# Kernel tuning notes

Hardware: AMD Instinct MI355X
Metric: run time of the kernel (lower is better)

The kernel has to match this reference:

```python
import jax, jax.numpy as jnp
import numpy as np
from itertools import permutations

# Static config (matches init_kwargs)
K = 4          # subgraph size; permdim P = (K-1)! = 6
H = 64         # hid_dim
B = 16         # number of graphs
N = 64         # nodes per graph (Nm == N)
SUBG_PER = 128 # subgraphs per graph
NS = B * SUBG_PER
OUT = 1
NREG = 4


def make_allperm(k):
    # all permutations of [1..k-1], with a 0 column prepended, transposed -> (k, P)
    perms = np.array(list(permutations(range(1, k))), dtype=np.int32)  # (P, k-1)
    allperm = np.concatenate([np.zeros((perms.shape[0], 1), np.int32), perms], axis=1)
    return jnp.asarray(allperm.T)  # (k, P)


def layer_norm(x, g, b, eps=1e-5):
    m = jnp.mean(x, axis=-1, keepdims=True)
    v = jnp.mean((x - m) ** 2, axis=-1, keepdims=True)
    return (x - m) / jnp.sqrt(v + eps) * g + b


def setup_inputs() -> dict:
    key = jax.random.key(0)
    ks = jax.random.split(key, 24)
    s = 1.0 / np.sqrt(H)
    # distinct node indices per subgraph: top-k of a random permutation
    r = jax.random.uniform(ks[2], (NS, N))
    subgs = jnp.argsort(r, axis=1)[:, :K].astype(jnp.int32)  # (NS, K)
    return {
        "x": jax.random.normal(ks[0], (B, N, 1), jnp.float32),
        "adj": (jax.random.uniform(ks[1], (B, N, N)) < 0.2).astype(jnp.float32),
        "subgs": subgs,
        "num_subg": jnp.full((B,), SUBG_PER, jnp.int32),
        # inmlp params (dead compute in original forward, kept for faithfulness)
        "in_w1": jax.random.normal(ks[3], (1, H)) * s,
        "in_b1": jnp.zeros((H,)),
        "in_w2": jax.random.normal(ks[4], (H, H)) * s,
        "in_b2": jnp.zeros((H,)),
        "in_ln_g": jnp.ones((H,)),
        "in_ln_b": jnp.zeros((H,)),
        "idemb": jax.random.normal(ks[5], (K + 2, H)) * 1.0,
        "id_w": jax.random.normal(ks[6], (H, H)) * s,
        "id_b": jnp.zeros((H,)),
        "set1_w": jax.random.normal(ks[7], (H, H)) * s,
        "set1_b": jnp.zeros((H,)),
        "set2_w": jax.random.normal(ks[8], (H, H)) * s,
        "set2_b": jnp.zeros((H,)),
        "reg_w1": jax.random.normal(ks[9], (NREG, H, H)) * s,
        "reg_b1": jnp.zeros((NREG, H)),
        "reg_w2": jax.random.normal(ks[10], (NREG, H, H)) * s,
        "reg_b2": jnp.zeros((NREG, H)),
        "reg_ln_g": jnp.ones((NREG, H)),
        "reg_ln_b": jnp.zeros((NREG, H)),
        "out_w": jax.random.normal(ks[11], (H, OUT)) * s,
        "out_b": jnp.zeros((OUT,)),
    }


def reference(x, adj, subgs, num_subg, in_w1, in_b1, in_w2, in_b2, in_ln_g, in_ln_b,
              idemb, id_w, id_b, set1_w, set1_b, set2_w, set2_b,
              reg_w1, reg_b1, reg_w2, reg_b2, reg_ln_g, reg_ln_b, out_w, out_b):
    b, n = adj.shape[0], adj.shape[-1]
    ns, k = subgs.shape
    h = idemb.shape[1]
    subgbatch = jnp.repeat(jnp.arange(b), num_subg, total_repeat_length=ns)  # (ns,)

    # inmlp (output is discarded by the original forward; only its shape is used)
    xe = jax.nn.relu(x @ in_w1 + in_b1)
    xe = jax.nn.relu(layer_norm(xe @ in_w2 + in_b2, in_ln_g, in_ln_b))
    del xe

    # node-id label injection: z[s, subgs[s, j], p, :] = emb(allperm[j, p]) * (j+1)*1000
    allperm = make_allperm(k)                                  # (k, P)
    p = allperm.shape[1]
    lab = idemb[allperm] * ((jnp.arange(k) + 1.0) * 1000.0)[:, None, None]  # (k, P, h)
    z = jnp.ones((ns, n, p, h), x.dtype)
    z = z.at[jnp.arange(ns)[:, None], subgs].set(jnp.broadcast_to(lab, (ns, k, p, h)))

    adj_ = adj[subgbatch]                                      # (ns, N, N)

    # id message-passing layer(s): z += SELU(Linear(A @ z)) ; num_layer_id = 1
    m = jnp.einsum('bij,bjpd->bipd', adj_, z)                  # (ns, N, P, h)
    z = z + jax.nn.selu(m @ id_w + id_b)

    z = jax.nn.selu(z.sum(axis=2) @ set1_w + set1_b)           # pool perms -> (ns, N, h)
    # num_layer_global = 0: no global message-passing layers
    g = jax.nn.selu(z.sum(axis=1) @ set2_w + set2_b)           # pool nodes -> (ns, h)
    g = jax.ops.segment_max(g, subgbatch, num_segments=b)      # global max pool -> (B, h)

    for i in range(reg_w1.shape[0]):
        t = jax.nn.relu(g @ reg_w1[i] + reg_b1[i])
        t = jax.nn.relu(layer_norm(t @ reg_w2[i] + reg_b2[i], reg_ln_g[i], reg_ln_b[i]))
        g = g + t
    return g @ out_w + out_b                                   # (B, out_dim)
```

## Files before the change

### kernel.cpp

```cpp
#include <hip/hip_runtime.h>
#include <math.h>

#define NB     16
#define NN     64
#define KK     4
#define PP     6
#define HH     64
#define NSUB   2048
#define NC0    65
#define NMASK  16
#define NCOMBO (NC0*NMASK)
#define NVAR   5

#define OFF_ROWSUM 0
#define OFF_LABW   1024
#define OFF_W1SUM  2560
#define OFF_BASEW  2624
#define OFF_T2     2944
#define OFF_GKEYS  335744

__device__ __constant__ int d_ap[4][6] = {
    {0,0,0,0,0,0},{1,1,2,2,3,3},{2,3,1,3,1,2},{3,2,3,1,2,1}};

static __device__ inline float selu_f(float x) {
    const float alpha = 1.6732632423543772f;
    const float scale = 1.0507009873554805f;
    return x > 0.0f ? scale * x : scale * alpha * expm1f(x);
}
static __device__ inline unsigned enc_f(float x) {
    unsigned b = __float_as_uint(x);
    return (b & 0x80000000u) ? ~b : (b | 0x80000000u);
}
static __device__ inline float dec_f(unsigned k) {
    unsigned b = (k & 0x80000000u) ? (k & 0x7FFFFFFFu) : ~k;
    return __uint_as_float(b);
}

__global__ __launch_bounds__(64) void k_prep(
    const float* __restrict__ adj, const float* __restrict__ idemb,
    const float* __restrict__ id_w, const float* __restrict__ set1_w,
    const float* __restrict__ set1_b, float* __restrict__ ws)
{
    const int t = threadIdx.x;
    const int blk = blockIdx.x;
    if (blk < NB) {
        const float4* row = reinterpret_cast<const float4*>(adj + (blk*NN + t)*NN);
        float s = 0.f;
        #pragma unroll
        for (int k = 0; k < 16; ++k) { float4 v = row[k]; s += v.x + v.y + v.z + v.w; }
        ws[OFF_ROWSUM + blk*NN + t] = s;
        return;
    }
    if (blk > NB) {
        const int jp = blk - NB - 1;
        const int j = jp / PP, p = jp % PP;
        const float sc = (float)(j+1) * 1000.0f;
        const float* er = idemb + d_ap[j][p]*HH;
        float s = 0.f;
        #pragma unroll
        for (int h = 0; h < HH; ++h) s += (er[h] * sc) * id_w[h*HH + t];
        ws[OFF_LABW + jp*HH + t] = s;
        return;
    }
    float* w1sum = ws + OFF_W1SUM;
    float* baseW = ws + OFF_BASEW;
    unsigned* gk = reinterpret_cast<unsigned*>(ws) + OFF_GKEYS;
    {
        float s = 0.f;
        for (int h = 0; h < HH; ++h) s += id_w[h*HH + t];
        w1sum[t] = s;
    }
    __shared__ float lsum[KK][HH];
    for (int j = 0; j < KK; ++j) {
        const float sc = (float)(j+1) * 1000.0f;
        float s = 0.f;
        for (int p = 0; p < PP; ++p) s += idemb[d_ap[j][p]*HH + t];
        lsum[j][t] = s * sc;
    }
    __syncthreads();
    {
        float cs = 0.f;
        for (int hp = 0; hp < HH; ++hp) cs += set1_w[hp*HH + t];
        baseW[t] = 6.0f * cs + set1_b[t];
        for (int j = 0; j < KK; ++j) {
            float d = 0.f;
            for (int hp = 0; hp < HH; ++hp) d += lsum[j][hp] * set1_w[hp*HH + t];
            baseW[(1+j)*HH + t] = d + set1_b[t];
        }
    }
    for (int i = t; i < NB*HH; i += 64) gk[i] = 0u;
}

__global__ __launch_bounds__(64) void k_table(
    const float* __restrict__ id_b, const float* __restrict__ set1_w,
    float* __restrict__ ws)
{
    const int c0   = blockIdx.x >> 4;
    const int mask = blockIdx.x & 15;
    const int t = threadIdx.x;
    const float* labW  = ws + OFF_LABW;
    const float* w1sum = ws + OFF_W1SUM;
    const float* baseW = ws + OFF_BASEW;
    const float fc0 = (float)c0;
    float acc = 0.f;
    #pragma unroll
    for (int p = 0; p < PP; ++p) {
        float arg = fc0 * w1sum[t] + id_b[t];
        #pragma unroll
        for (int j = 0; j < KK; ++j)
            if ((mask >> j) & 1) arg += labW[(j*PP + p)*HH + t];
        acc += selu_f(arg);
    }
    __shared__ float S[HH];
    S[t] = acc;
    __syncthreads();
    float o = 0.f;
    #pragma unroll
    for (int hp = 0; hp < HH; ++hp) o += S[hp] * set1_w[hp*HH + t];
    #pragma unroll
    for (int var = 0; var < NVAR; ++var)
        ws[OFF_T2 + (var*NCOMBO + blockIdx.x)*HH + t] = selu_f(o + baseW[var*HH + t]);
}

__global__ __launch_bounds__(256) void k_main(
    const float* __restrict__ adj, const int* __restrict__ subgs,
    const float* __restrict__ set2_w, const float* __restrict__ set2_b,
    float* __restrict__ ws)
{
    const int s = blockIdx.x;
    const int b = s >> 7;
    __shared__ int sub[KK];
    __shared__ float gpart[4][HH];
    if (threadIdx.x < KK) sub[threadIdx.x] = subgs[s*KK + threadIdx.x];
    __syncthreads();
    const int w = threadIdx.x >> 6, h = threadIdx.x & 63;
    const int s0 = sub[0], s1 = sub[1], s2 = sub[2], s3 = sub[3];
    const float* adjb = adj + b*NN*NN;
    const float* rs   = ws + OFF_ROWSUM + b*NN;
    const float* T2   = ws + OFF_T2;
    float facc = 0.f;
    #pragma unroll 4
    for (int it = 0; it < 16; ++it) {
        const int i = w*16 + it;
        const float* arow = adjb + i*NN;
        const float a0 = arow[s0], a1 = arow[s1], a2 = arow[s2], a3 = arow[s3];
        const float c0f = rs[i] - (a0 + a1 + a2 + a3);
        const int ic0 = (int)(c0f + 0.5f);
        const int mask = (a0 != 0.f ? 1 : 0) | (a1 != 0.f ? 2 : 0)
                       | (a2 != 0.f ? 4 : 0) | (a3 != 0.f ? 8 : 0);
        const int var = (i==s0) ? 1 : (i==s1) ? 2 : (i==s2) ? 3 : (i==s3) ? 4 : 0;
        facc += T2[(var*NCOMBO + ic0*NMASK + mask)*HH + h];
    }
    gpart[w][h] = facc;
    __syncthreads();
    if (w == 0) gpart[0][h] = gpart[0][h] + gpart[1][h] + gpart[2][h] + gpart[3][h];
    __syncthreads();
    if (w == 0) {
        float o = set2_b[h];
        #pragma unroll
        for (int hp = 0; hp < HH; ++hp)
            o += gpart[0][hp] * set2_w[hp*HH + h];
        const float gq = selu_f(o);
        unsigned* gk = reinterpret_cast<unsigned*>(ws) + OFF_GKEYS;
        atomicMax(gk + b*HH + h, enc_f(gq));
    }
}

__global__ __launch_bounds__(256) void k_head(
    const float* __restrict__ reg_w1, const float* __restrict__ reg_b1,
    const float* __restrict__ reg_w2, const float* __restrict__ reg_b2,
    const float* __restrict__ reg_ln_g, const float* __restrict__ reg_ln_b,
    const float* __restrict__ out_w, const float* __restrict__ out_b,
    const float* __restrict__ ws, float* __restrict__ out)
{
    __shared__ float swgt[2*KK*HH*HH];
    __shared__ float gs[HH];
    const int tid = threadIdx.x;
    {
        const float4* g1 = reinterpret_cast<const float4*>(reg_w1);
        const float4* g2 = reinterpret_cast<const float4*>(reg_w2);
        float4* s4 = reinterpret_cast<float4*>(swgt);
        #pragma unroll
        for (int i = 0; i < 16; ++i) s4[i*256 + tid] = g1[i*256 + tid];
        #pragma unroll
        for (int i = 0; i < 16; ++i) s4[4096 + i*256 + tid] = g2[i*256 + tid];
    }
    __syncthreads();
    if (tid >= 64) return;
    const int r = blockIdx.x;
    const int h = tid;
    const unsigned* gk = reinterpret_cast<const unsigned*>(ws) + OFF_GKEYS;
    float g = dec_f(gk[r*HH + h]);
    for (int blk = 0; blk < 4; ++blk) {
        const float* w1 = swgt + blk*HH*HH;
        const float* w2 = swgt + KK*HH*HH + blk*HH*HH;
        gs[h] = g;
        __syncthreads();
        float t1 = reg_b1[blk*HH + h];
        #pragma unroll
        for (int hp = 0; hp < HH; ++hp) t1 += gs[hp] * w1[hp*HH + h];
        t1 = fmaxf(t1, 0.f);
        gs[h] = t1;
        __syncthreads();
        float u = reg_b2[blk*HH + h];
        #pragma unroll
        for (int hp = 0; hp < HH; ++hp) u += gs[hp] * w2[hp*HH + h];
        __syncthreads();
        float m = u;
        #pragma unroll
        for (int d = 1; d < 64; d <<= 1) m += __shfl_xor(m, d, 64);
        m *= (1.0f/64.0f);
        const float dv = u - m;
        float v = dv * dv;
        #pragma unroll
        for (int d = 1; d < 64; d <<= 1) v += __shfl_xor(v, d, 64);
        v *= (1.0f/64.0f);
        const float y = dv / sqrtf(v + 1e-5f) * reg_ln_g[blk*HH + h] + reg_ln_b[blk*HH + h];
        g += fmaxf(y, 0.f);
    }
    float pr = g * out_w[h];
    #pragma unroll
    for (int d = 1; d < 64; d <<= 1) pr += __shfl_xor(pr, d, 64);
    if (h == 0) out[r] = pr + out_b[0];
}

extern "C" void kernel_launch(void* const* d_in, const int* in_sizes, int n_in,
                              void* d_out, int out_size, void* d_ws, size_t ws_size,
                              hipStream_t stream)
{
    const float* adj     = (const float*)d_in[1];
    const int*   subgs   = (const int*)  d_in[2];
    const float* idemb   = (const float*)d_in[10];
    const float* id_w    = (const float*)d_in[11];
    const float* id_b    = (const float*)d_in[12];
    const float* set1_w  = (const float*)d_in[13];
    const float* set1_b  = (const float*)d_in[14];
    const float* set2_w  = (const float*)d_in[15];
    const float* set2_b  = (const float*)d_in[16];
    const float* reg_w1  = (const float*)d_in[17];
    const float* reg_b1  = (const float*)d_in[18];
    const float* reg_w2  = (const float*)d_in[19];
    const float* reg_b2  = (const float*)d_in[20];
    const float* reg_lng = (const float*)d_in[21];
    const float* reg_lnb = (const float*)d_in[22];
    const float* out_w   = (const float*)d_in[23];
    const float* out_b   = (const float*)d_in[24];
    float* ws  = (float*)d_ws;
    float* out = (float*)d_out;

    hipLaunchKernelGGL(k_prep,  dim3(NB + 1 + KK*PP), dim3(64),  0, stream,
                       adj, idemb, id_w, set1_w, set1_b, ws);
    hipLaunchKernelGGL(k_table, dim3(NCOMBO), dim3(64),   0, stream,
                       id_b, set1_w, ws);
    hipLaunchKernelGGL(k_main,  dim3(NSUB),   dim3(256),  0, stream,
                       adj, subgs, set2_w, set2_b, ws);
    hipLaunchKernelGGL(k_head,  dim3(NB),     dim3(256),  0, stream,
                       reg_w1, reg_b1, reg_w2, reg_b2, reg_lng, reg_lnb,
                       out_w, out_b, ws, out);
}
```

Measured before the change: 140.1 us.

## Fuse prep, table and main kernels into one cooperative kernel with grid syncs

Merges the three launches (prep, lookup-table build, per-subgraph main) into one cooperative kernel of 512 blocks that uses grid-wide syncs between phases. Each block handles four subgraphs in a loop. The aim is to remove kernel launch gaps and inter-kernel drain/fill overhead. The cost is grid.sync barriers and fewer blocks for the main phase. If the cooperative launch fails, it falls back to the original three kernels.

After: 283.0 us. 2.02x slower.

```diff
diff --git a/kernel.cpp b/kernel.cpp
--- a/kernel.cpp
+++ b/kernel.cpp
@@ -1,5 +1,8 @@
 #include <hip/hip_runtime.h>
+#include <hip/hip_cooperative_groups.h>
 #include <math.h>
+
+namespace cg = cooperative_groups;
 
 #define NB     16
 #define NN     64
@@ -11,6 +14,7 @@
 #define NMASK  16
 #define NCOMBO (NC0*NMASK)
 #define NVAR   5
+#define GRID_F 512
 
 #define OFF_ROWSUM 0
 #define OFF_LABW   1024
@@ -34,6 +38,137 @@
 static __device__ inline float dec_f(unsigned k) {
     unsigned b = (k & 0x80000000u) ? (k & 0x7FFFFFFFu) : ~k;
     return __uint_as_float(b);
+}
+
+__global__ __launch_bounds__(256, 4) void k_fused(
+    const float* __restrict__ adj, const int* __restrict__ subgs,
+    const float* __restrict__ idemb, const float* __restrict__ id_w,
+    const float* __restrict__ id_b, const float* __restrict__ set1_w,
+    const float* __restrict__ set1_b, const float* __restrict__ set2_w,
+    const float* __restrict__ set2_b, float* __restrict__ ws)
+{
+    cg::grid_group grid = cg::this_grid();
+    const int g   = blockIdx.x;
+    const int tid = threadIdx.x;
+    const int w   = tid >> 6, h = tid & 63;
+    __shared__ int   sub[KK];
+    __shared__ float gpart[4][HH];
+
+    if (g < NB) {
+        if (tid < 64) {
+            const float4* row = reinterpret_cast<const float4*>(adj + (g*NN + tid)*NN);
+            float s = 0.f;
+            #pragma unroll
+            for (int k = 0; k < 16; ++k) { float4 v = row[k]; s += v.x + v.y + v.z + v.w; }
+            ws[OFF_ROWSUM + g*NN + tid] = s;
+        }
+    } else if (g < NB + KK*PP) {
+        if (tid < 64) {
+            const int jp = g - NB;
+            const int j = jp / PP, p = jp % PP;
+            const float sc = (float)(j+1) * 1000.0f;
+            const float* er = idemb + d_ap[j][p]*HH;
+            float s = 0.f;
+            #pragma unroll
+            for (int hh = 0; hh < HH; ++hh) s += (er[hh] * sc) * id_w[hh*HH + tid];
+            ws[OFF_LABW + jp*HH + tid] = s;
+        }
+    } else if (g == NB + KK*PP) {
+        if (tid < 64) {
+            float s = 0.f;
+            for (int hh = 0; hh < HH; ++hh) s += id_w[hh*HH + tid];
+            ws[OFF_W1SUM + tid] = s;
+        }
+    } else if (g < NB + KK*PP + 1 + NVAR) {
+        if (tid < 64) {
+            const int var = g - (NB + KK*PP + 1);
+            if (var == 0) {
+                float cs = 0.f;
+                for (int hp = 0; hp < HH; ++hp) cs += set1_w[hp*HH + tid];
+                ws[OFF_BASEW + tid] = 6.0f * cs + set1_b[tid];
+            } else {
+                const int j = var - 1;
+                const float sc = (float)(j+1) * 1000.0f;
+                float l = 0.f;
+                #pragma unroll
+                for (int p = 0; p < PP; ++p) l += idemb[d_ap[j][p]*HH + tid];
+                l *= sc;
+                float d = 0.f;
+                #pragma unroll
+                for (int hp = 0; hp < HH; ++hp) d += __shfl(l, hp, 64) * set1_w[hp*HH + tid];
+                ws[OFF_BASEW + var*HH + tid] = d + set1_b[tid];
+            }
+        }
+    } else if (g == NB + KK*PP + 1 + NVAR) {
+        if (tid < 64) {
+            unsigned* gk = reinterpret_cast<unsigned*>(ws) + OFF_GKEYS;
+            for (int i = tid; i < NB*HH; i += 64) gk[i] = 0u;
+        }
+    }
+    grid.sync();
+
+    if (g < NCOMBO/4) {
+        const int c = g*4 + w;
+        const int c0 = c >> 4, mask = c & 15;
+        const float* labW  = ws + OFF_LABW;
+        const float* w1sum = ws + OFF_W1SUM;
+        const float* baseW = ws + OFF_BASEW;
+        const float fc0 = (float)c0;
+        float acc = 0.f;
+        #pragma unroll
+        for (int p = 0; p < PP; ++p) {
+            float arg = fc0 * w1sum[h] + id_b[h];
+            #pragma unroll
+            for (int j = 0; j < KK; ++j)
+                if ((mask >> j) & 1) arg += labW[(j*PP + p)*HH + h];
+            acc += selu_f(arg);
+        }
+        float o = 0.f;
+        #pragma unroll
+        for (int hp = 0; hp < HH; ++hp) o += __shfl(acc, hp, 64) * set1_w[hp*HH + h];
+        #pragma unroll
+        for (int var = 0; var < NVAR; ++var)
+            ws[OFF_T2 + (var*NCOMBO + c)*HH + h] = selu_f(o + baseW[var*HH + h]);
+    }
+    grid.sync();
+
+    const float* T2 = ws + OFF_T2;
+    #pragma unroll
+    for (int ss = 0; ss < NSUB/GRID_F; ++ss) {
+        const int s = g + ss*GRID_F;
+        const int b = s >> 7;
+        if (tid < KK) sub[tid] = subgs[s*KK + tid];
+        __syncthreads();
+        const int s0 = sub[0], s1 = sub[1], s2 = sub[2], s3 = sub[3];
+        const float* adjb = adj + b*NN*NN;
+        const float* rs   = ws + OFF_ROWSUM + b*NN;
+        float facc = 0.f;
+        #pragma unroll 4
+        for (int it = 0; it < 16; ++it) {
+            const int i = w*16 + it;
+            const float* arow = adjb + i*NN;
+            const float a0 = arow[s0], a1 = arow[s1], a2 = arow[s2], a3 = arow[s3];
+            const float c0f = rs[i] - (a0 + a1 + a2 + a3);
+            const int ic0 = (int)(c0f + 0.5f);
+            const int mask = (a0 != 0.f ? 1 : 0) | (a1 != 0.f ? 2 : 0)
+                           | (a2 != 0.f ? 4 : 0) | (a3 != 0.f ? 8 : 0);
+            const int var = (i==s0) ? 1 : (i==s1) ? 2 : (i==s2) ? 3 : (i==s3) ? 4 : 0;
+            facc += T2[(var*NCOMBO + ic0*NMASK + mask)*HH + h];
+        }
+        gpart[w][h] = facc;
+        __syncthreads();
+        if (w == 0) {
+            const float gsum = gpart[0][h] + gpart[1][h] + gpart[2][h] + gpart[3][h];
+            float o = set2_b[h];
+            #pragma unroll
+            for (int hp = 0; hp < HH; ++hp)
+                o += __shfl(gsum, hp, 64) * set2_w[hp*HH + h];
+            const float gq = selu_f(o);
+            unsigned* gk = reinterpret_cast<unsigned*>(ws) + OFF_GKEYS;
+            atomicMax(gk + b*HH + h, enc_f(gq));
+        }
+        __syncthreads();
+    }
 }
 
 __global__ __launch_bounds__(64) void k_prep(
@@ -248,13 +383,20 @@
     float* ws  = (float*)d_ws;
     float* out = (float*)d_out;
 
-    hipLaunchKernelGGL(k_prep,  dim3(NB + 1 + KK*PP), dim3(64),  0, stream,
-                       adj, idemb, id_w, set1_w, set1_b, ws);
-    hipLaunchKernelGGL(k_table, dim3(NCOMBO), dim3(64),   0, stream,
-                       id_b, set1_w, ws);
-    hipLaunchKernelGGL(k_main,  dim3(NSUB),   dim3(256),  0, stream,
-                       adj, subgs, set2_w, set2_b, ws);
-    hipLaunchKernelGGL(k_head,  dim3(NB),     dim3(256),  0, stream,
+    void* args[] = { (void*)&adj, (void*)&subgs, (void*)&idemb, (void*)&id_w,
+                     (void*)&id_b, (void*)&set1_w, (void*)&set1_b,
+                     (void*)&set2_w, (void*)&set2_b, (void*)&ws };
+    hipError_t ce = hipLaunchCooperativeKernel((void*)k_fused, dim3(GRID_F),
+                                               dim3(256), args, 0, stream);
+    if (ce != hipSuccess) {
+        hipLaunchKernelGGL(k_prep,  dim3(NB + 1 + KK*PP), dim3(64), 0, stream,
+                           adj, idemb, id_w, set1_w, set1_b, ws);
+        hipLaunchKernelGGL(k_table, dim3(NCOMBO), dim3(64),  0, stream,
+                           id_b, set1_w, ws);
+        hipLaunchKernelGGL(k_main,  dim3(NSUB),   dim3(256), 0, stream,
+                           adj, subgs, set2_w, set2_b, ws);
+    }
+    hipLaunchKernelGGL(k_head, dim3(NB), dim3(256), 0, stream,
                        reg_w1, reg_b1, reg_w2, reg_b2, reg_lng, reg_lnb,
                        out_w, out_b, ws, out);
 }
```

## Fuse prep into table kernel, recompute row sums in main, batch two subgraphs per block

Applied to the files above, without the earlier changes.

Removes the separate k_prep launch. Each table block now recomputes its own label projections, w1 column sums and base terms, using wave shuffles in place of shared memory. Row sums of adj move into k_main, and each k_main block now handles two subgraphs, which halves the grid and reuses the row sums. This saves one launch and a global round trip, but every table block repeats the redundant 64x64 dot products, up to 24 of them plus the base terms.

Result: slower. 190.0 us (+35.6%).

```diff
diff --git a/kernel.cpp b/kernel.cpp
--- a/kernel.cpp
+++ b/kernel.cpp
@@ -12,12 +12,8 @@
 #define NCOMBO (NC0*NMASK)
 #define NVAR   5
 
-#define OFF_ROWSUM 0
-#define OFF_LABW   1024
-#define OFF_W1SUM  2560
-#define OFF_BASEW  2624
-#define OFF_T2     2944
-#define OFF_GKEYS  335744
+#define OFF_T2     0
+#define OFF_GKEYS  332800
 
 __device__ __constant__ int d_ap[4][6] = {
     {0,0,0,0,0,0},{1,1,2,2,3,3},{2,3,1,3,1,2},{3,2,3,1,2,1}};
@@ -36,90 +32,75 @@
     return __uint_as_float(b);
 }
 
-__global__ __launch_bounds__(64) void k_prep(
-    const float* __restrict__ adj, const float* __restrict__ idemb,
-    const float* __restrict__ id_w, const float* __restrict__ set1_w,
+__global__ __launch_bounds__(64) void k_tableX(
+    const float* __restrict__ idemb, const float* __restrict__ id_w,
+    const float* __restrict__ id_b, const float* __restrict__ set1_w,
     const float* __restrict__ set1_b, float* __restrict__ ws)
 {
+    const int c = blockIdx.x;
+    const int c0 = c >> 4, mask = c & 15;
     const int t = threadIdx.x;
-    const int blk = blockIdx.x;
-    if (blk < NB) {
-        const float4* row = reinterpret_cast<const float4*>(adj + (blk*NN + t)*NN);
-        float s = 0.f;
-        #pragma unroll
-        for (int k = 0; k < 16; ++k) { float4 v = row[k]; s += v.x + v.y + v.z + v.w; }
-        ws[OFF_ROWSUM + blk*NN + t] = s;
-        return;
-    }
-    if (blk > NB) {
-        const int jp = blk - NB - 1;
-        const int j = jp / PP, p = jp % PP;
-        const float sc = (float)(j+1) * 1000.0f;
-        const float* er = idemb + d_ap[j][p]*HH;
-        float s = 0.f;
-        #pragma unroll
-        for (int h = 0; h < HH; ++h) s += (er[h] * sc) * id_w[h*HH + t];
-        ws[OFF_LABW + jp*HH + t] = s;
-        return;
-    }
-    float* w1sum = ws + OFF_W1SUM;
-    float* baseW = ws + OFF_BASEW;
-    unsigned* gk = reinterpret_cast<unsigned*>(ws) + OFF_GKEYS;
-    {
-        float s = 0.f;
-        for (int h = 0; h < HH; ++h) s += id_w[h*HH + t];
-        w1sum[t] = s;
-    }
-    __shared__ float lsum[KK][HH];
+
+    if (c == 0) {
+        unsigned* gk = reinterpret_cast<unsigned*>(ws) + OFF_GKEYS;
+        for (int i = t; i < NB*HH; i += 64) gk[i] = 0u;
+    }
+
+    float w1s = 0.f;
+    for (int hh = 0; hh < HH; ++hh) w1s += id_w[hh*HH + t];
+
+    float labw[KK][PP];
+    #pragma unroll
     for (int j = 0; j < KK; ++j) {
-        const float sc = (float)(j+1) * 1000.0f;
-        float s = 0.f;
-        for (int p = 0; p < PP; ++p) s += idemb[d_ap[j][p]*HH + t];
-        lsum[j][t] = s * sc;
-    }
-    __syncthreads();
+        if ((mask >> j) & 1) {
+            const float sc = (float)(j+1) * 1000.0f;
+            #pragma unroll
+            for (int p = 0; p < PP; ++p) {
+                const float* er = idemb + d_ap[j][p]*HH;
+                float s = 0.f;
+                for (int hh = 0; hh < HH; ++hh) s += (er[hh] * sc) * id_w[hh*HH + t];
+                labw[j][p] = s;
+            }
+        }
+    }
+
+    const float fc0 = (float)c0;
+    float acc = 0.f;
+    #pragma unroll
+    for (int p = 0; p < PP; ++p) {
+        float arg = fc0 * w1s + id_b[t];
+        #pragma unroll
+        for (int j = 0; j < KK; ++j)
+            if ((mask >> j) & 1) arg += labw[j][p];
+        acc += selu_f(arg);
+    }
+
+    float o = 0.f;
+    #pragma unroll
+    for (int hp = 0; hp < HH; ++hp) o += __shfl(acc, hp, 64) * set1_w[hp*HH + t];
+
+    float bw[NVAR];
     {
         float cs = 0.f;
         for (int hp = 0; hp < HH; ++hp) cs += set1_w[hp*HH + t];
-        baseW[t] = 6.0f * cs + set1_b[t];
-        for (int j = 0; j < KK; ++j) {
-            float d = 0.f;
-            for (int hp = 0; hp < HH; ++hp) d += lsum[j][hp] * set1_w[hp*HH + t];
-            baseW[(1+j)*HH + t] = d + set1_b[t];
-        }
-    }
-    for (int i = t; i < NB*HH; i += 64) gk[i] = 0u;
-}
-
-__global__ __launch_bounds__(64) void k_table(
-    const float* __restrict__ id_b, const float* __restrict__ set1_w,
-    float* __restrict__ ws)
-{
-    const int c0   = blockIdx.x >> 4;
-    const int mask = blockIdx.x & 15;
-    const int t = threadIdx.x;
-    const float* labW  = ws + OFF_LABW;
-    const float* w1sum = ws + OFF_W1SUM;
-    const float* baseW = ws + OFF_BASEW;
-    const float fc0 = (float)c0;
-    float acc = 0.f;
-    #pragma unroll
-    for (int p = 0; p < PP; ++p) {
-        float arg = fc0 * w1sum[t] + id_b[t];
-        #pragma unroll
-        for (int j = 0; j < KK; ++j)
-            if ((mask >> j) & 1) arg += labW[(j*PP + p)*HH + t];
-        acc += selu_f(arg);
-    }
-    __shared__ float S[HH];
-    S[t] = acc;
-    __syncthreads();
-    float o = 0.f;
-    #pragma unroll
-    for (int hp = 0; hp < HH; ++hp) o += S[hp] * set1_w[hp*HH + t];
+        bw[0] = 6.0f * cs + set1_b[t];
+    }
+    #pragma unroll
+    for (int j = 0; j < KK; ++j) {
+        const float sc = (float)(j+1) * 1000.0f;
+        float l = 0.f;
+        #pragma unroll
+        for (int p = 0; p < PP; ++p) l += idemb[d_ap[j][p]*HH + t];
+        l *= sc;
+        float d = 0.f;
+        #pragma unroll
+        for (int hp = 0; hp < HH; ++hp) d += __shfl(l, hp, 64) * set1_w[hp*HH + t];
+        bw[1+j] = d + set1_b[t];
+    }
+
     #pragma unroll
     for (int var = 0; var < NVAR; ++var)
-        ws[OFF_T2 + (var*NCOMBO + blockIdx.x)*HH + t] = selu_f(o + baseW[var*HH + t]);
+        ws[OFF_T2 + (var*NCOMBO + c)*HH + t] = selu_f(o + bw[var]);
 }
 
 __global__ __launch_bounds__(256) void k_main(
@@ -127,42 +108,56 @@
     const float* __restrict__ set2_w, const float* __restrict__ set2_b,
     float* __restrict__ ws)
 {
-    const int s = blockIdx.x;
-    const int b = s >> 7;
-    __shared__ int sub[KK];
+    const int g = blockIdx.x;
+    const int b = g >> 6;
+    const int tid = threadIdx.x;
+    const int w = tid >> 6, h = tid & 63;
+    __shared__ float rs_s[NN];
+    __shared__ int   sub[KK];
     __shared__ float gpart[4][HH];
-    if (threadIdx.x < KK) sub[threadIdx.x] = subgs[s*KK + threadIdx.x];
-    __syncthreads();
-    const int w = threadIdx.x >> 6, h = threadIdx.x & 63;
-    const int s0 = sub[0], s1 = sub[1], s2 = sub[2], s3 = sub[3];
+
+    if (tid < 64) {
+        const float4* row = reinterpret_cast<const float4*>(adj + (b*NN + tid)*NN);
+        float s = 0.f;
+        #pragma unroll
+        for (int k = 0; k < 16; ++k) { float4 v = row[k]; s += v.x + v.y + v.z + v.w; }
+        rs_s[tid] = s;
+    }
     const float* adjb = adj + b*NN*NN;
-    const float* rs   = ws + OFF_ROWSUM + b*NN;
     const float* T2   = ws + OFF_T2;
-    float facc = 0.f;
-    #pragma unroll 4
-    for (int it = 0; it < 16; ++it) {
-        const int i = w*16 + it;
-        const float* arow = adjb + i*NN;
-        const float a0 = arow[s0], a1 = arow[s1], a2 = arow[s2], a3 = arow[s3];
-        const float c0f = rs[i] - (a0 + a1 + a2 + a3);
-        const int ic0 = (int)(c0f + 0.5f);
-        const int mask = (a0 != 0.f ? 1 : 0) | (a1 != 0.f ? 2 : 0)
-                       | (a2 != 0.f ? 4 : 0) | (a3 != 0.f ? 8 : 0);
-        const int var = (i==s0) ? 1 : (i==s1) ? 2 : (i==s2) ? 3 : (i==s3) ? 4 : 0;
-        facc += T2[(var*NCOMBO + ic0*NMASK + mask)*HH + h];
-    }
-    gpart[w][h] = facc;
-    __syncthreads();
-    if (w == 0) gpart[0][h] = gpart[0][h] + gpart[1][h] + gpart[2][h] + gpart[3][h];
-    __syncthreads();
-    if (w == 0) {
-        float o = set2_b[h];
-        #pragma unroll
-        for (int hp = 0; hp < HH; ++hp)
-            o += gpart[0][hp] * set2_w[hp*HH + h];
-        const float gq = selu_f(o);
-        unsigned* gk = reinterpret_cast<unsigned*>(ws) + OFF_GKEYS;
-        atomicMax(gk + b*HH + h, enc_f(gq));
+    unsigned* gk = reinterpret_cast<unsigned*>(ws) + OFF_GKEYS;
+
+    #pragma unroll
+    for (int ss = 0; ss < 2; ++ss) {
+        const int s = g*2 + ss;
+        if (tid < KK) sub[tid] = subgs[s*KK + tid];
+        __syncthreads();
+        const int s0 = sub[0], s1 = sub[1], s2 = sub[2], s3 = sub[3];
+        float facc = 0.f;
+        #pragma unroll 4
+        for (int it = 0; it < 16; ++it) {
+            const int i = w*16 + it;
+            const float* arow = adjb + i*NN;
+            const float a0 = arow[s0], a1 = arow[s1], a2 = arow[s2], a3 = arow[s3];
+            const float c0f = rs_s[i] - (a0 + a1 + a2 + a3);
+            const int ic0 = (int)(c0f + 0.5f);
+            const int mask = (a0 != 0.f ? 1 : 0) | (a1 != 0.f ? 2 : 0)
+                           | (a2 != 0.f ? 4 : 0) | (a3 != 0.f ? 8 : 0);
+            const int var = (i==s0) ? 1 : (i==s1) ? 2 : (i==s2) ? 3 : (i==s3) ? 4 : 0;
+            facc += T2[(var*NCOMBO + ic0*NMASK + mask)*HH + h];
+        }
+        gpart[w][h] = facc;
+        __syncthreads();
+        if (w == 0) {
+            const float gsum = gpart[0][h] + gpart[1][h] + gpart[2][h] + gpart[3][h];
+            float o = set2_b[h];
+            #pragma unroll
+            for (int hp = 0; hp < HH; ++hp)
+                o += __shfl(gsum, hp, 64) * set2_w[hp*HH + h];
+            const float gq = selu_f(o);
+            atomicMax(gk + b*HH + h, enc_f(gq));
+        }
+        __syncthreads();
     }
 }
 
@@ -248,13 +243,11 @@
     float* ws  = (float*)d_ws;
     float* out = (float*)d_out;
 
-    hipLaunchKernelGGL(k_prep,  dim3(NB + 1 + KK*PP), dim3(64),  0, stream,
-                       adj, idemb, id_w, set1_w, set1_b, ws);
-    hipLaunchKernelGGL(k_table, dim3(NCOMBO), dim3(64),   0, stream,
-                       id_b, set1_w, ws);
-    hipLaunchKernelGGL(k_main,  dim3(NSUB),   dim3(256),  0, stream,
+    hipLaunchKernelGGL(k_tableX, dim3(NCOMBO), dim3(64),  0, stream,
+                       idemb, id_w, id_b, set1_w, set1_b, ws);
+    hipLaunchKernelGGL(k_main,   dim3(NSUB/2), dim3(256), 0, stream,
                        adj, subgs, set2_w, set2_b, ws);
-    hipLaunchKernelGGL(k_head,  dim3(NB),     dim3(256),  0, stream,
+    hipLaunchKernelGGL(k_head,   dim3(NB),     dim3(256), 0, stream,
                        reg_w1, reg_b1, reg_w2, reg_b2, reg_lng, reg_lnb,
                        out_w, out_b, ws, out);
 }
```
